# Kernel tuning notes

Hardware: AMD Instinct MI355X
Metric: run time of the kernel (lower is better)

The kernel has to match this reference:

```python
import jax, jax.numpy as jnp
import numpy as np

N, E, D, H, L, G = 50000, 800000, 128, 8, 3, 64
C = D // H  # per-head dim


def setup_inputs() -> dict:
    key = jax.random.key(0)
    ks = jax.random.split(key, 10)
    s = 1.0 / np.sqrt(D)  # glorot-ish scale
    return {
        "x": jax.random.normal(ks[0], (N, D), jnp.float32),
        "edge_index": jax.random.randint(ks[1], (2, E), 0, N, jnp.int32),
        "batch": jnp.sort(jax.random.randint(ks[2], (N,), 0, G, jnp.int32)),
        "Wq": jax.random.normal(ks[3], (L, D, D), jnp.float32) * s,
        "bq": jnp.zeros((L, D), jnp.float32),
        "Wk": jax.random.normal(ks[4], (L, D, D), jnp.float32) * s,
        "bk": jnp.zeros((L, D), jnp.float32),
        "Wv": jax.random.normal(ks[5], (L, D, D), jnp.float32) * s,
        "bv": jnp.zeros((L, D), jnp.float32),
        "Ws": jax.random.normal(ks[6], (L, D, D), jnp.float32) * s,
        "bs": jnp.zeros((L, D), jnp.float32),
        "w_gate": jax.random.normal(ks[7], (D, 1), jnp.float32) * s,
        "b_gate": jnp.zeros((1,), jnp.float32),
    }


def transformer_conv(x, src, dst, Wq, bq, Wk, bk, Wv, bv, Ws, bs):
    # PyG TransformerConv (concat=True, root_weight=True, no edge_attr, eval mode)
    n = x.shape[0]
    q = (x @ Wq + bq).reshape(n, H, C)
    k = (x @ Wk + bk).reshape(n, H, C)
    v = (x @ Wv + bv).reshape(n, H, C)
    # attention logits per edge: [E, H]
    alpha = jnp.einsum('ehc,ehc->eh', q[dst], k[src]) / np.sqrt(C).astype(np.float32)
    # segment softmax over incoming edges of each destination node
    amax = jax.ops.segment_max(alpha, dst, num_segments=n)          # [N, H]
    ea = jnp.exp(alpha - amax[dst])
    denom = jax.ops.segment_sum(ea, dst, num_segments=n)            # [N, H]
    attn = ea / (denom[dst] + 1e-16)                                # [E, H]
    msg = v[src] * attn[:, :, None]                                 # [E, H, C]
    out = jax.ops.segment_sum(msg, dst, num_segments=n).reshape(n, H * C)
    return out + x @ Ws + bs                                        # skip connection


def reference(x, edge_index, batch, Wq, bq, Wk, bk, Wv, bv, Ws, bs, w_gate, b_gate):
    src, dst = edge_index[0], edge_index[1]
    for l in range(L):
        x = transformer_conv(x, src, dst, Wq[l], bq[l], Wk[l], bk[l],
                             Wv[l], bv[l], Ws[l], bs[l])
    # ReadoutPhase: gated sum pool || max pool
    score = jax.nn.sigmoid(x @ w_gate + b_gate)                     # [N, 1]
    pool_sum = jax.ops.segment_sum(score * x, batch, num_segments=G)
    pool_max = jax.ops.segment_max(x, batch, num_segments=G)
    return jnp.concatenate([pool_sum, pool_max], axis=1)            # [G, 2D]
```

## Files before the change

### kernel.cpp

```cpp
#include <hip/hip_runtime.h>
#include <hip/hip_bf16.h>

#define NN 50000
#define EE 800000
#define GG 64
#define PCH 16
#define SCB ((NN + 255) / 256)

typedef __attribute__((ext_vector_type(8)))  short          s16x8;
typedef __attribute__((ext_vector_type(8)))  unsigned short u16x8;
typedef __attribute__((ext_vector_type(16))) float          f32x16;

union BFU { __hip_bfloat16 h; unsigned short u; };
__device__ __forceinline__ unsigned short f2bf(float f) {
    BFU b; b.h = __float2bfloat16(f); return b.u;
}
#define B2F_LO(u) __uint_as_float((u) << 16)
#define B2F_HI(u) __uint_as_float((u) & 0xffff0000u)
#define BF2F(us)  __uint_as_float(((unsigned)(us)) << 16)

__global__ __launch_bounds__(256) void hist_kernel(const int* __restrict__ dst,
                                                   int* __restrict__ counts) {
    int e = blockIdx.x * 256 + threadIdx.x;
    if (e < EE) atomicAdd(&counts[dst[e]], 1);
}

__global__ __launch_bounds__(256)
void block_scan_deg(const int* __restrict__ counts, int* __restrict__ offsets,
                    int* __restrict__ bsums, int* __restrict__ dhist) {
    __shared__ int sm[256];
    __shared__ int lh[256];
    const int t = threadIdx.x;
    const int i = blockIdx.x * 256 + t;
    const int v = (i < NN) ? counts[i] : 0;
    lh[t] = 0;
    sm[t] = v;
    __syncthreads();
    if (i < NN) atomicAdd(&lh[min(v, 255)], 1);
    for (int off = 1; off < 256; off <<= 1) {
        int val = (t >= off) ? sm[t - off] : 0;
        __syncthreads();
        sm[t] += val;
        __syncthreads();
    }
    if (i < NN) offsets[i] = sm[t] - v;
    if (t == 255) bsums[blockIdx.x] = sm[255];
    if (lh[t]) atomicAdd(&dhist[t], lh[t]);
}

__global__ __launch_bounds__(256)
void scan2(int* __restrict__ bsums, int* __restrict__ dhist) {
    int* arr = (blockIdx.x == 0) ? bsums : dhist;
    const int lim = (blockIdx.x == 0) ? SCB : 256;
    __shared__ int sm[256];
    const int t = threadIdx.x;
    const int v = (t < lim) ? arr[t] : 0;
    sm[t] = v;
    __syncthreads();
    for (int off = 1; off < 256; off <<= 1) {
        int val = (t >= off) ? sm[t - off] : 0;
        __syncthreads();
        sm[t] += val;
        __syncthreads();
    }
    if (t < lim) arr[t] = sm[t] - v;
}

__global__ __launch_bounds__(256)
void add_base_starts(int* __restrict__ offsets, const int* __restrict__ bsums,
                     const int* __restrict__ batch, int* __restrict__ starts) {
    const int i = blockIdx.x * 256 + threadIdx.x;
    if (i < NN) offsets[i] += bsums[blockIdx.x];
    if (i == 0) offsets[NN] = EE;
    if (i <= NN) {
        int b  = (i < NN) ? batch[i] : GG;
        int bp = (i == 0) ? -1 : batch[i - 1];
        for (int g = bp + 1; g <= b && g <= GG; ++g) starts[g] = i;
    }
}

__global__ __launch_bounds__(256)
void deg_scatter(const int* __restrict__ counts, const int* __restrict__ dbase,
                 int* __restrict__ dcur, int* __restrict__ perm) {
    __shared__ int lh[256];
    __shared__ int lb[256];
    const int t = threadIdx.x;
    lh[t] = 0;
    __syncthreads();
    const int i = blockIdx.x * 256 + t;
    int d = 0, r = 0;
    if (i < NN) {
        d = min(counts[i], 255);
        r = atomicAdd(&lh[d], 1);
    }
    __syncthreads();
    if (lh[t]) lb[t] = atomicAdd(&dcur[t], lh[t]);
    __syncthreads();
    if (i < NN) perm[dbase[d] + lb[d] + r] = i;
}

__global__ __launch_bounds__(256) void scatter_kernel(const int* __restrict__ src,
                                                      const int* __restrict__ dst,
                                                      const int* __restrict__ offs,
                                                      int* __restrict__ cursor,
                                                      int* __restrict__ csrc) {
    int e = blockIdx.x * 256 + threadIdx.x;
    if (e < EE) {
        int dn = dst[e];
        int p = atomicAdd(&cursor[dn], 1);
        csrc[offs[dn] + p] = src[e];
    }
}

__global__ __launch_bounds__(256)
void prep_weights(const float* __restrict__ Wq, const float* __restrict__ Wk,
                  const float* __restrict__ Wv, const float* __restrict__ Ws,
                  unsigned short* __restrict__ wfh, unsigned short* __restrict__ wfl) {
    const int mat = blockIdx.x;
    const int l = mat >> 2, m = mat & 3;
    const float* W;
    switch (m) {
        case 0:  W = Wq; break;
        case 1:  W = Wk; break;
        case 2:  W = Wv; break;
        default: W = Ws; break;
    }
    W += (size_t)l * 16384;
    const int t = threadIdx.x;
    const int col = blockIdx.y * 16 + (t >> 4);
    const int kk  = t & 15;
    u16x8 hi, lo;
    #pragma unroll
    for (int j = 0; j < 8; ++j) {
        float w = W[(kk * 8 + j) * 128 + col];
        unsigned short uh = f2bf(w);
        hi[j] = uh;
        lo[j] = f2bf(w - BF2F(uh));
    }
    const size_t o = (size_t)mat * 16384 + ((size_t)kk * 128 + col) * 8;
    *(u16x8*)(wfh + o) = hi;
    *(u16x8*)(wfl + o) = lo;
}

__global__ __launch_bounds__(256)
void gemm_mfma(const float* __restrict__ xin,
               const unsigned short* __restrict__ wHg,
               const unsigned short* __restrict__ wLg,
               const float* __restrict__ bq, const float* __restrict__ bk,
               const float* __restrict__ bv, const float* __restrict__ bs,
               float* __restrict__ q, unsigned short* __restrict__ kvb,
               float* __restrict__ xs) {
    __shared__ unsigned short xl[16384];
    const int t = threadIdx.x;
    const int n0 = blockIdx.x * 64;

    const float4* X4 = (const float4*)xin;
    for (int i = t; i < 1024; i += 256) {
        const int row = i >> 4, ch = i & 15;
        const int node = n0 + row;
        float4 fa = make_float4(0.f, 0.f, 0.f, 0.f);
        float4 fb = make_float4(0.f, 0.f, 0.f, 0.f);
        if (node < NN) { fa = X4[node * 32 + ch * 2]; fb = X4[node * 32 + ch * 2 + 1]; }
        const float fv[8] = {fa.x, fa.y, fa.z, fa.w, fb.x, fb.y, fb.z, fb.w};
        u16x8 hi, lo;
        #pragma unroll
        for (int j = 0; j < 8; ++j) {
            unsigned short uh = f2bf(fv[j]);
            hi[j] = uh;
            lo[j] = f2bf(fv[j] - BF2F(uh));
        }
        const int base = row * 128 + (ch ^ (row & 7)) * 8;
        *(u16x8*)&xl[base] = hi;
        *(u16x8*)&xl[8192 + base] = lo;
    }
    __syncthreads();

    const int lane = t & 63, wid = t >> 6;
    const int r = lane & 31, g = lane >> 5;
    const int nt = (wid & 1) * 32;
    const int cb = (wid >> 1) * 64;
    s16x8 ah[8], al[8];
    {
        const int row = nt + r;
        const int s = row & 7;
        const int rb = row * 128;
        #pragma unroll
        for (int kc = 0; kc < 8; ++kc) {
            const int idx = rb + (((kc << 1) | g) ^ s) * 8;
            ah[kc] = *(const s16x8*)&xl[idx];
            al[kc] = *(const s16x8*)&xl[8192 + idx];
        }
    }
    const int col0 = cb + r, col1 = cb + 32 + r;

    #pragma unroll
    for (int pm = 0; pm < 2; ++pm) {
        const int m = pm ? 3 : 0;
        const unsigned short* WH = wHg + m * 16384;
        const unsigned short* WL = wLg + m * 16384;
        f32x16 acc0, acc1;
        #pragma unroll
        for (int j = 0; j < 16; ++j) { acc0[j] = 0.f; acc1[j] = 0.f; }
        #pragma unroll
        for (int kc = 0; kc < 8; ++kc) {
            const int kk = (kc << 1) | g;
            const s16x8 b0 = *(const s16x8*)&WH[(kk * 128 + col0) * 8];
            const s16x8 b1 = *(const s16x8*)&WH[(kk * 128 + col1) * 8];
            const s16x8 c0 = *(const s16x8*)&WL[(kk * 128 + col0) * 8];
            const s16x8 c1 = *(const s16x8*)&WL[(kk * 128 + col1) * 8];
            acc0 = __builtin_amdgcn_mfma_f32_32x32x16_bf16(ah[kc], b0, acc0, 0, 0, 0);
            acc1 = __builtin_amdgcn_mfma_f32_32x32x16_bf16(ah[kc], b1, acc1, 0, 0, 0);
            acc0 = __builtin_amdgcn_mfma_f32_32x32x16_bf16(al[kc], b0, acc0, 0, 0, 0);
            acc1 = __builtin_amdgcn_mfma_f32_32x32x16_bf16(al[kc], b1, acc1, 0, 0, 0);
            acc0 = __builtin_amdgcn_mfma_f32_32x32x16_bf16(ah[kc], c0, acc0, 0, 0, 0);
            acc1 = __builtin_amdgcn_mfma_f32_32x32x16_bf16(ah[kc], c1, acc1, 0, 0, 0);
        }
        const float* bp = pm ? bs : bq;
        float* outp = pm ? xs : q;
        const float b0 = bp[col0], b1 = bp[col1];
        #pragma unroll
        for (int reg = 0; reg < 16; ++reg) {
            const int node = n0 + nt + (reg & 3) + 8 * (reg >> 2) + 4 * g;
            if (node < NN) {
                outp[node * 128 + col0] = acc0[reg] + b0;
                outp[node * 128 + col1] = acc1[reg] + b1;
            }
        }
    }

    {
        const unsigned short* WK = wHg + 1 * 16384;
        const unsigned short* WV = wHg + 2 * 16384;
        f32x16 ak0, ak1, av0, av1;
        #pragma unroll
        for (int j = 0; j < 16; ++j) { ak0[j] = 0.f; ak1[j] = 0.f; av0[j] = 0.f; av1[j] = 0.f; }
        #pragma unroll
        for (int kc = 0; kc < 8; ++kc) {
            const int kk = (kc << 1) | g;
            const s16x8 k0 = *(const s16x8*)&WK[(kk * 128 + col0) * 8];
            const s16x8 k1 = *(const s16x8*)&WK[(kk * 128 + col1) * 8];
            const s16x8 v0 = *(const s16x8*)&WV[(kk * 128 + col0) * 8];
            const s16x8 v1 = *(const s16x8*)&WV[(kk * 128 + col1) * 8];
            ak0 = __builtin_amdgcn_mfma_f32_32x32x16_bf16(ah[kc], k0, ak0, 0, 0, 0);
            ak1 = __builtin_amdgcn_mfma_f32_32x32x16_bf16(ah[kc], k1, ak1, 0, 0, 0);
            av0 = __builtin_amdgcn_mfma_f32_32x32x16_bf16(ah[kc], v0, av0, 0, 0, 0);
            av1 = __builtin_amdgcn_mfma_f32_32x32x16_bf16(ah[kc], v1, av1, 0, 0, 0);
        }
        const float bk0 = bk[col0], bk1 = bk[col1];
        const float bv0 = bv[col0], bv1 = bv[col1];
        const int k0o = (col0 >> 4) * 32 + (col0 & 15);
        const int k1o = (col1 >> 4) * 32 + (col1 & 15);
        #pragma unroll
        for (int reg = 0; reg < 16; ++reg) {
            const int node = n0 + nt + (reg & 3) + 8 * (reg >> 2) + 4 * g;
            if (node < NN) {
                unsigned short* row = kvb + (size_t)node * 256;
                row[k0o]      = f2bf(ak0[reg] + bk0);
                row[k1o]      = f2bf(ak1[reg] + bk1);
                row[k0o + 16] = f2bf(av0[reg] + bv0);
                row[k1o + 16] = f2bf(av1[reg] + bv1);
            }
        }
    }
}

__global__ __launch_bounds__(256)
void attn_kernel(const float* __restrict__ q, const uint4* __restrict__ kv4,
                 float* __restrict__ xio,
                 const int* __restrict__ offs, const int* __restrict__ csrc,
                 const int* __restrict__ perm) {
    const int t = threadIdx.x;
    const int h = t & 7;
    const int quarter = (t >> 3) & 3;
    const int idx = blockIdx.x * 8 + (t >> 5);
    const int n = perm[NN - 1 - idx];
    const float4* qp = (const float4*)(q + n * 128 + h * 16);
    const float4 q0 = qp[0], q1 = qp[1], q2 = qp[2], q3 = qp[3];
    float m = -__builtin_inff();
    float d = 0.f;
    float4 a0 = {}, a1 = {}, a2 = {}, a3 = {};
    const int e0 = offs[n], e1 = offs[n + 1];
    const int estart = e0 + quarter;
    if (estart < e1) {
        uint4 ka, kb, va, vb;
        { const uint4* p = kv4 + (size_t)csrc[estart] * 32 + h * 4;
          ka = p[0]; kb = p[1]; va = p[2]; vb = p[3]; }
        uint4 na, nb, nc, nd;
        if (estart + 4 < e1) {
            const uint4* p = kv4 + (size_t)csrc[estart + 4] * 32 + h * 4;
            na = p[0]; nb = p[1]; nc = p[2]; nd = p[3];
        }
        for (int ec = estart; ec < e1; ec += 4) {
            uint4 fa, fb, fc, fd;
            if (ec + 8 < e1) {
                const uint4* p = kv4 + (size_t)csrc[ec + 8] * 32 + h * 4;
                fa = p[0]; fb = p[1]; fc = p[2]; fd = p[3];
            }
            float dot =
                q0.x * B2F_LO(ka.x) + q0.y * B2F_HI(ka.x) + q0.z * B2F_LO(ka.y) + q0.w * B2F_HI(ka.y)
              + q1.x * B2F_LO(ka.z) + q1.y * B2F_HI(ka.z) + q1.z * B2F_LO(ka.w) + q1.w * B2F_HI(ka.w)
              + q2.x * B2F_LO(kb.x) + q2.y * B2F_HI(kb.x) + q2.z * B2F_LO(kb.y) + q2.w * B2F_HI(kb.y)
              + q3.x * B2F_LO(kb.z) + q3.y * B2F_HI(kb.z) + q3.z * B2F_LO(kb.w) + q3.w * B2F_HI(kb.w);
            const float alpha = dot * 0.25f;
            const float nm = fmaxf(m, alpha);
            const float scale = __expf(m - nm);
            const float p = __expf(alpha - nm);
            d = d * scale + p;
            a0.x = a0.x * scale + p * B2F_LO(va.x); a0.y = a0.y * scale + p * B2F_HI(va.x);
            a0.z = a0.z * scale + p * B2F_LO(va.y); a0.w = a0.w * scale + p * B2F_HI(va.y);
            a1.x = a1.x * scale + p * B2F_LO(va.z); a1.y = a1.y * scale + p * B2F_HI(va.z);
            a1.z = a1.z * scale + p * B2F_LO(va.w); a1.w = a1.w * scale + p * B2F_HI(va.w);
            a2.x = a2.x * scale + p * B2F_LO(vb.x); a2.y = a2.y * scale + p * B2F_HI(vb.x);
            a2.z = a2.z * scale + p * B2F_LO(vb.y); a2.w = a2.w * scale + p * B2F_HI(vb.y);
            a3.x = a3.x * scale + p * B2F_LO(vb.z); a3.y = a3.y * scale + p * B2F_HI(vb.z);
            a3.z = a3.z * scale + p * B2F_LO(vb.w); a3.w = a3.w * scale + p * B2F_HI(vb.w);
            m = nm;
            ka = na; kb = nb; va = nc; vb = nd;
            na = fa; nb = fb; nc = fc; nd = fd;
        }
    }
    #pragma unroll
    for (int o = 8; o <= 16; o <<= 1) {
        const float mp = __shfl_xor(m, o);
        const float dp = __shfl_xor(d, o);
        const float mc = fmaxf(fmaxf(m, mp), -1e30f);
        const float s0 = __expf(m - mc);
        const float s1 = __expf(mp - mc);
        d = d * s0 + dp * s1;
        float pa;
        pa = __shfl_xor(a0.x, o); a0.x = a0.x * s0 + pa * s1;
        pa = __shfl_xor(a0.y, o); a0.y = a0.y * s0 + pa * s1;
        pa = __shfl_xor(a0.z, o); a0.z = a0.z * s0 + pa * s1;
        pa = __shfl_xor(a0.w, o); a0.w = a0.w * s0 + pa * s1;
        pa = __shfl_xor(a1.x, o); a1.x = a1.x * s0 + pa * s1;
        pa = __shfl_xor(a1.y, o); a1.y = a1.y * s0 + pa * s1;
        pa = __shfl_xor(a1.z, o); a1.z = a1.z * s0 + pa * s1;
        pa = __shfl_xor(a1.w, o); a1.w = a1.w * s0 + pa * s1;
        pa = __shfl_xor(a2.x, o); a2.x = a2.x * s0 + pa * s1;
        pa = __shfl_xor(a2.y, o); a2.y = a2.y * s0 + pa * s1;
        pa = __shfl_xor(a2.z, o); a2.z = a2.z * s0 + pa * s1;
        pa = __shfl_xor(a2.w, o); a2.w = a2.w * s0 + pa * s1;
        pa = __shfl_xor(a3.x, o); a3.x = a3.x * s0 + pa * s1;
        pa = __shfl_xor(a3.y, o); a3.y = a3.y * s0 + pa * s1;
        pa = __shfl_xor(a3.z, o); a3.z = a3.z * s0 + pa * s1;
        pa = __shfl_xor(a3.w, o); a3.w = a3.w * s0 + pa * s1;
        m = mc;
    }
    if (quarter == 0) {
        const float inv = 1.f / (d + 1e-16f);
        float4* op = (float4*)(xio + n * 128 + h * 16);
        float4 o0 = op[0], o1 = op[1], o2 = op[2], o3 = op[3];
        o0.x += a0.x * inv; o0.y += a0.y * inv; o0.z += a0.z * inv; o0.w += a0.w * inv;
        o1.x += a1.x * inv; o1.y += a1.y * inv; o1.z += a1.z * inv; o1.w += a1.w * inv;
        o2.x += a2.x * inv; o2.y += a2.y * inv; o2.z += a2.z * inv; o2.w += a2.w * inv;
        o3.x += a3.x * inv; o3.y += a3.y * inv; o3.z += a3.z * inv; o3.w += a3.w * inv;
        op[0] = o0; op[1] = o1; op[2] = o2; op[3] = o3;
    }
}

__global__ __launch_bounds__(128)
void pool_partial(const float* __restrict__ x, const float* __restrict__ wg,
                  const float* __restrict__ bg, const int* __restrict__ starts,
                  float* __restrict__ psum, float* __restrict__ pmax) {
    const int g  = blockIdx.x / PCH;
    const int ch = blockIdx.x % PCH;
    const int c  = threadIdx.x;
    const int s0 = starts[g], s1 = starts[g + 1];
    const int total = s1 - s0;
    const int len = (total + PCH - 1) / PCH;
    const int n0 = s0 + ch * len;
    const int n1 = min(n0 + len, s1);
    const float w = wg[c];
    const float b = bg[0];
    __shared__ float red[2];
    float sum = 0.f, mx = -__builtin_inff();
    for (int n = n0; n < n1; ++n) {
        const float xv = x[n * 128 + c];
        float p = xv * w;
        #pragma unroll
        for (int o = 32; o; o >>= 1) p += __shfl_xor(p, o);
        if ((c & 63) == 0) red[c >> 6] = p;
        __syncthreads();
        const float dot = red[0] + red[1];
        __syncthreads();
        const float score = 1.f / (1.f + __expf(-(dot + b)));
        sum += score * xv;
        mx = fmaxf(mx, xv);
    }
    psum[blockIdx.x * 128 + c] = sum;
    pmax[blockIdx.x * 128 + c] = mx;
}

__global__ __launch_bounds__(128)
void pool_final(const float* __restrict__ psum, const float* __restrict__ pmax,
                float* __restrict__ out) {
    const int g = blockIdx.x, c = threadIdx.x;
    float s = 0.f, m = -__builtin_inff();
    #pragma unroll
    for (int ch = 0; ch < PCH; ++ch) {
        s += psum[(g * PCH + ch) * 128 + c];
        m = fmaxf(m, pmax[(g * PCH + ch) * 128 + c]);
    }
    out[g * 256 + c] = s;
    out[g * 256 + 128 + c] = m;
}

extern "C" void kernel_launch(void* const* d_in, const int* in_sizes, int n_in,
                              void* d_out, int out_size, void* d_ws, size_t ws_size,
                              hipStream_t stream) {
    const float* x     = (const float*)d_in[0];
    const int*   ei    = (const int*)d_in[1];
    const int*   batch = (const int*)d_in[2];
    const float* Wq = (const float*)d_in[3];
    const float* bq = (const float*)d_in[4];
    const float* Wk = (const float*)d_in[5];
    const float* bk = (const float*)d_in[6];
    const float* Wv = (const float*)d_in[7];
    const float* bv = (const float*)d_in[8];
    const float* Ws = (const float*)d_in[9];
    const float* bs = (const float*)d_in[10];
    const float* wg = (const float*)d_in[11];
    const float* bg = (const float*)d_in[12];
    float* out = (float*)d_out;

    char* w = (char*)d_ws;
    float* qb            = (float*)w;          w += (size_t)NN * 128 * 4;
    unsigned short* kvb  = (unsigned short*)w; w += (size_t)NN * 256 * 2;
    float* bufA          = (float*)w;          w += (size_t)NN * 128 * 4;
    float* bufB          = (float*)w;          w += (size_t)NN * 128 * 4;
    float* psum          = (float*)w;          w += (size_t)GG * PCH * 128 * 4;
    float* pmax          = (float*)w;          w += (size_t)GG * PCH * 128 * 4;
    unsigned short* wfh  = (unsigned short*)w; w += (size_t)12 * 16384 * 2;
    unsigned short* wfl  = (unsigned short*)w; w += (size_t)12 * 16384 * 2;
    int* counts          = (int*)w;            w += (size_t)NN * 4;
    int* cursor          = (int*)w;            w += (size_t)NN * 4;
    int* dhist           = (int*)w;            w += (size_t)256 * 4;
    int* dcur            = (int*)w;            w += (size_t)256 * 4;
    const size_t zero_bytes = (size_t)(NN + NN + 256 + 256) * 4;
    int* offsets         = (int*)w;            w += (size_t)(NN + 1) * 4;
    int* bsums           = (int*)w;            w += (size_t)256 * 4;
    int* perm            = (int*)w;            w += (size_t)NN * 4;
    int* csrc            = (int*)w;            w += (size_t)EE * 4;
    int* starts          = (int*)w;            w += (size_t)(GG + 1) * 4;

    const int* srcI = ei;
    const int* dstI = ei + EE;

    hipMemsetAsync(counts, 0, zero_bytes, stream);
    hist_kernel<<<(EE + 255) / 256, 256, 0, stream>>>(dstI, counts);
    block_scan_deg<<<SCB, 256, 0, stream>>>(counts, offsets, bsums, dhist);
    scan2<<<2, 256, 0, stream>>>(bsums, dhist);
    add_base_starts<<<SCB, 256, 0, stream>>>(offsets, bsums, batch, starts);
    deg_scatter<<<SCB, 256, 0, stream>>>(counts, dhist, dcur, perm);
    scatter_kernel<<<(EE + 255) / 256, 256, 0, stream>>>(srcI, dstI, offsets, cursor, csrc);
    prep_weights<<<dim3(12, 8), 256, 0, stream>>>(Wq, Wk, Wv, Ws, wfh, wfl);

    const float* xin = x;
    float* bufs[2] = {bufA, bufB};
    const int gemmBlocks = (NN + 63) / 64;
    const int attnBlocks = NN / 8;
    for (int l = 0; l < 3; ++l) {
        float* xs = bufs[l & 1];
        gemm_mfma<<<gemmBlocks, 256, 0, stream>>>(
            xin, wfh + (size_t)l * 4 * 16384, wfl + (size_t)l * 4 * 16384,
            bq + (size_t)l * 128, bk + (size_t)l * 128,
            bv + (size_t)l * 128, bs + (size_t)l * 128,
            qb, kvb, xs);
        attn_kernel<<<attnBlocks, 256, 0, stream>>>(qb, (const uint4*)kvb, xs, offsets, csrc, perm);
        xin = xs;
    }

    pool_partial<<<GG * PCH, 128, 0, stream>>>(xin, wg, bg, starts, psum, pmax);
    pool_final<<<GG, 128, 0, stream>>>(psum, pmax, out);
}
```

Baseline: 442.5 us.

## Store Q in bf16, drop degree-sorted node permutation, and collapse CSR prep kernels

Q projections are now written and read as bf16 instead of fp32, halving that buffer's write and read traffic. The attention kernel now walks nodes in natural order instead of through a degree-sorted permutation, which removes the degree histogram and scatter kernels. The multi-kernel scan is replaced by a single kernel that claims per-block bases with a global atomic, and edge ends come from counts. In exchange, CSR segments are no longer in node order, Q loses precision, and the degree-based load balancing across blocks is gone.

```diff
diff --git a/kernel.cpp b/kernel.cpp
--- a/kernel.cpp
+++ b/kernel.cpp
@@ -26,35 +26,14 @@
 }
 
 __global__ __launch_bounds__(256)
-void block_scan_deg(const int* __restrict__ counts, int* __restrict__ offsets,
-                    int* __restrict__ bsums, int* __restrict__ dhist) {
+void node_prep(const int* __restrict__ counts, int* __restrict__ offsets,
+               int* __restrict__ gcur,
+               const int* __restrict__ batch, int* __restrict__ starts) {
     __shared__ int sm[256];
-    __shared__ int lh[256];
+    __shared__ int base;
     const int t = threadIdx.x;
     const int i = blockIdx.x * 256 + t;
     const int v = (i < NN) ? counts[i] : 0;
-    lh[t] = 0;
-    sm[t] = v;
-    __syncthreads();
-    if (i < NN) atomicAdd(&lh[min(v, 255)], 1);
-    for (int off = 1; off < 256; off <<= 1) {
-        int val = (t >= off) ? sm[t - off] : 0;
-        __syncthreads();
-        sm[t] += val;
-        __syncthreads();
-    }
-    if (i < NN) offsets[i] = sm[t] - v;
-    if (t == 255) bsums[blockIdx.x] = sm[255];
-    if (lh[t]) atomicAdd(&dhist[t], lh[t]);
-}
-
-__global__ __launch_bounds__(256)
-void scan2(int* __restrict__ bsums, int* __restrict__ dhist) {
-    int* arr = (blockIdx.x == 0) ? bsums : dhist;
-    const int lim = (blockIdx.x == 0) ? SCB : 256;
-    __shared__ int sm[256];
-    const int t = threadIdx.x;
-    const int v = (t < lim) ? arr[t] : 0;
     sm[t] = v;
     __syncthreads();
     for (int off = 1; off < 256; off <<= 1) {
@@ -63,40 +42,14 @@
         sm[t] += val;
         __syncthreads();
     }
-    if (t < lim) arr[t] = sm[t] - v;
-}
-
-__global__ __launch_bounds__(256)
-void add_base_starts(int* __restrict__ offsets, const int* __restrict__ bsums,
-                     const int* __restrict__ batch, int* __restrict__ starts) {
-    const int i = blockIdx.x * 256 + threadIdx.x;
-    if (i < NN) offsets[i] += bsums[blockIdx.x];
-    if (i == 0) offsets[NN] = EE;
+    if (t == 255) base = atomicAdd(gcur, sm[255]);
+    __syncthreads();
+    if (i < NN) offsets[i] = base + sm[t] - v;
     if (i <= NN) {
         int b  = (i < NN) ? batch[i] : GG;
         int bp = (i == 0) ? -1 : batch[i - 1];
         for (int g = bp + 1; g <= b && g <= GG; ++g) starts[g] = i;
     }
-}
-
-__global__ __launch_bounds__(256)
-void deg_scatter(const int* __restrict__ counts, const int* __restrict__ dbase,
-                 int* __restrict__ dcur, int* __restrict__ perm) {
-    __shared__ int lh[256];
-    __shared__ int lb[256];
-    const int t = threadIdx.x;
-    lh[t] = 0;
-    __syncthreads();
-    const int i = blockIdx.x * 256 + t;
-    int d = 0, r = 0;
-    if (i < NN) {
-        d = min(counts[i], 255);
-        r = atomicAdd(&lh[d], 1);
-    }
-    __syncthreads();
-    if (lh[t]) lb[t] = atomicAdd(&dcur[t], lh[t]);
-    __syncthreads();
-    if (i < NN) perm[dbase[d] + lb[d] + r] = i;
 }
 
 __global__ __launch_bounds__(256) void scatter_kernel(const int* __restrict__ src,
@@ -148,7 +101,7 @@
                const unsigned short* __restrict__ wLg,
                const float* __restrict__ bq, const float* __restrict__ bk,
                const float* __restrict__ bv, const float* __restrict__ bs,
-               float* __restrict__ q, unsigned short* __restrict__ kvb,
+               unsigned short* __restrict__ qbf, unsigned short* __restrict__ kvb,
                float* __restrict__ xs) {
     __shared__ unsigned short xl[16384];
     const int t = threadIdx.x;
@@ -216,14 +169,25 @@
             acc1 = __builtin_amdgcn_mfma_f32_32x32x16_bf16(ah[kc], c1, acc1, 0, 0, 0);
         }
         const float* bp = pm ? bs : bq;
-        float* outp = pm ? xs : q;
         const float b0 = bp[col0], b1 = bp[col1];
-        #pragma unroll
-        for (int reg = 0; reg < 16; ++reg) {
-            const int node = n0 + nt + (reg & 3) + 8 * (reg >> 2) + 4 * g;
-            if (node < NN) {
-                outp[node * 128 + col0] = acc0[reg] + b0;
-                outp[node * 128 + col1] = acc1[reg] + b1;
+        if (pm == 0) {
+            #pragma unroll
+            for (int reg = 0; reg < 16; ++reg) {
+                const int node = n0 + nt + (reg & 3) + 8 * (reg >> 2) + 4 * g;
+                if (node < NN) {
+                    unsigned short* qrow = qbf + (size_t)node * 128;
+                    qrow[col0] = f2bf(acc0[reg] + b0);
+                    qrow[col1] = f2bf(acc1[reg] + b1);
+                }
+            }
+        } else {
+            #pragma unroll
+            for (int reg = 0; reg < 16; ++reg) {
+                const int node = n0 + nt + (reg & 3) + 8 * (reg >> 2) + 4 * g;
+                if (node < NN) {
+                    xs[node * 128 + col0] = acc0[reg] + b0;
+                    xs[node * 128 + col1] = acc1[reg] + b1;
+                }
             }
         }
     }
@@ -265,21 +229,24 @@
 }
 
 __global__ __launch_bounds__(256)
-void attn_kernel(const float* __restrict__ q, const uint4* __restrict__ kv4,
+void attn_kernel(const unsigned short* __restrict__ qbf, const uint4* __restrict__ kv4,
                  float* __restrict__ xio,
-                 const int* __restrict__ offs, const int* __restrict__ csrc,
-                 const int* __restrict__ perm) {
+                 const int* __restrict__ offs, const int* __restrict__ cnts,
+                 const int* __restrict__ csrc) {
     const int t = threadIdx.x;
     const int h = t & 7;
     const int quarter = (t >> 3) & 3;
-    const int idx = blockIdx.x * 8 + (t >> 5);
-    const int n = perm[NN - 1 - idx];
-    const float4* qp = (const float4*)(q + n * 128 + h * 16);
-    const float4 q0 = qp[0], q1 = qp[1], q2 = qp[2], q3 = qp[3];
+    const int n = blockIdx.x * 8 + (t >> 5);
+    const uint4* qp = (const uint4*)(qbf + (size_t)n * 128) + h * 2;
+    const uint4 qA = qp[0], qB = qp[1];
+    const float4 q0 = make_float4(B2F_LO(qA.x), B2F_HI(qA.x), B2F_LO(qA.y), B2F_HI(qA.y));
+    const float4 q1 = make_float4(B2F_LO(qA.z), B2F_HI(qA.z), B2F_LO(qA.w), B2F_HI(qA.w));
+    const float4 q2 = make_float4(B2F_LO(qB.x), B2F_HI(qB.x), B2F_LO(qB.y), B2F_HI(qB.y));
+    const float4 q3 = make_float4(B2F_LO(qB.z), B2F_HI(qB.z), B2F_LO(qB.w), B2F_HI(qB.w));
     float m = -__builtin_inff();
     float d = 0.f;
     float4 a0 = {}, a1 = {}, a2 = {}, a3 = {};
-    const int e0 = offs[n], e1 = offs[n + 1];
+    const int e0 = offs[n], e1 = e0 + cnts[n];
     const int estart = e0 + quarter;
     if (estart < e1) {
         uint4 ka, kb, va, vb;
@@ -348,7 +315,7 @@
     }
     if (quarter == 0) {
         const float inv = 1.f / (d + 1e-16f);
-        float4* op = (float4*)(xio + n * 128 + h * 16);
+        float4* op = (float4*)(xio + (size_t)n * 128 + h * 16);
         float4 o0 = op[0], o1 = op[1], o2 = op[2], o3 = op[3];
         o0.x += a0.x * inv; o0.y += a0.y * inv; o0.z += a0.z * inv; o0.w += a0.w * inv;
         o1.x += a1.x * inv; o1.y += a1.y * inv; o1.z += a1.z * inv; o1.w += a1.w * inv;
@@ -424,7 +391,7 @@
     float* out = (float*)d_out;
 
     char* w = (char*)d_ws;
-    float* qb            = (float*)w;          w += (size_t)NN * 128 * 4;
+    unsigned short* qbf  = (unsigned short*)w; w += (size_t)NN * 128 * 2;
     unsigned short* kvb  = (unsigned short*)w; w += (size_t)NN * 256 * 2;
     float* bufA          = (float*)w;          w += (size_t)NN * 128 * 4;
     float* bufB          = (float*)w;          w += (size_t)NN * 128 * 4;
@@ -434,12 +401,9 @@
     unsigned short* wfl  = (unsigned short*)w; w += (size_t)12 * 16384 * 2;
     int* counts          = (int*)w;            w += (size_t)NN * 4;
     int* cursor          = (int*)w;            w += (size_t)NN * 4;
-    int* dhist           = (int*)w;            w += (size_t)256 * 4;
-    int* dcur            = (int*)w;            w += (size_t)256 * 4;
-    const size_t zero_bytes = (size_t)(NN + NN + 256 + 256) * 4;
-    int* offsets         = (int*)w;            w += (size_t)(NN + 1) * 4;
-    int* bsums           = (int*)w;            w += (size_t)256 * 4;
-    int* perm            = (int*)w;            w += (size_t)NN * 4;
+    int* gcur            = (int*)w;            w += (size_t)64 * 4;
+    const size_t zero_bytes = (size_t)(NN + NN + 64) * 4;
+    int* offsets         = (int*)w;            w += (size_t)NN * 4;
     int* csrc            = (int*)w;            w += (size_t)EE * 4;
     int* starts          = (int*)w;            w += (size_t)(GG + 1) * 4;
 
@@ -448,10 +412,7 @@
 
     hipMemsetAsync(counts, 0, zero_bytes, stream);
     hist_kernel<<<(EE + 255) / 256, 256, 0, stream>>>(dstI, counts);
-    block_scan_deg<<<SCB, 256, 0, stream>>>(counts, offsets, bsums, dhist);
-    scan2<<<2, 256, 0, stream>>>(bsums, dhist);
-    add_base_starts<<<SCB, 256, 0, stream>>>(offsets, bsums, batch, starts);
-    deg_scatter<<<SCB, 256, 0, stream>>>(counts, dhist, dcur, perm);
+    node_prep<<<SCB, 256, 0, stream>>>(counts, offsets, gcur, batch, starts);
     scatter_kernel<<<(EE + 255) / 256, 256, 0, stream>>>(srcI, dstI, offsets, cursor, csrc);
     prep_weights<<<dim3(12, 8), 256, 0, stream>>>(Wq, Wk, Wv, Ws, wfh, wfl);
 
@@ -465,8 +426,8 @@
             xin, wfh + (size_t)l * 4 * 16384, wfl + (size_t)l * 4 * 16384,
             bq + (size_t)l * 128, bk + (size_t)l * 128,
             bv + (size_t)l * 128, bs + (size_t)l * 128,
-            qb, kvb, xs);
-        attn_kernel<<<attnBlocks, 256, 0, stream>>>(qb, (const uint4*)kvb, xs, offsets, csrc, perm);
+            qbf, kvb, xs);
+        attn_kernel<<<attnBlocks, 256, 0, stream>>>(qbf, (const uint4*)kvb, xs, offsets, counts, csrc);
         xin = xs;
     }
 
```

Measured after the change: 431.5 us. 2.5% less time.
